# Optimization experiments

Hardware: AMD Instinct MI355X
Metric: run time of the kernel (lower is better)

The kernel has to match this reference:

```python
import jax, jax.numpy as jnp
import numpy as np

B, T = 8, 32
DSENS, DA = 512, 32
DS = DE = DIM = 128  # dim_structure = dim_encoded_sensory = memory dim


def l2norm(x, eps=1e-12):
    return x / jnp.maximum(jnp.linalg.norm(x, axis=-1, keepdims=True), eps)


def mlp3(x, W1, b1, W2, b2, W3, b3):
    h = jax.nn.relu(x @ W1 + b1)
    h = jax.nn.relu(h @ W2 + b2)
    return h @ W3 + b3


def mse(a, b):
    return jnp.mean((a - b) ** 2)


def assoc_scan(x, gate, prev):
    # h_t = gate_t * h_{t-1} + x_t with h_0 = prev.  x:[b,t,w], gate:[b,t,1], prev:[b,w]
    x = x.at[:, 0].add(gate[:, 0] * prev)
    def combine(ca, cb):
        ga, xa = ca
        gb, xb = cb
        return ga * gb, xb + gb * xa
    _, h = jax.lax.associative_scan(combine, (gate, x), axis=1)
    return h


def _forward(sensory, actions, enc_w, dec_w, pi_w1, pi_b1, pi_w2, pi_b2, pi_w3, pi_b3,
             rnn_init_hidden, wq, wk, wv, w_hp, m_w1, m_b1, m_w2, m_b2, m_w3, m_b3,
             o_w1, o_b1, o_w2, o_b2, o_w3, o_b3, v_w1, v_b1, v_w2, v_b2, v_w3, v_b3,
             integration_ratio):
    b, t = actions.shape[:2]
    # --- path integration: action MLP -> per-step transition matrices -> sequential RNN scan ---
    trans = mlp3(actions, pi_w1, pi_b1, pi_w2, pi_b2, pi_w3, pi_b3).reshape(b, t, DS, DS)
    h0 = jnp.broadcast_to(l2norm(rnn_init_hidden)[0], (b, DS))
    def step(h, Tm):
        h = l2norm(jax.nn.relu(jnp.einsum('bi,bij->bj', h, Tm)))
        return h, h
    _, hs = jax.lax.scan(step, h0, jnp.moveaxis(trans, 1, 0))
    structural = jnp.moveaxis(hs, 0, 1)                      # [b,t,DS]

    enc = sensory @ enc_w                                    # [b,t,DE]
    meta_p = (m_w1, m_b1, m_w2, m_b2, m_w3, m_b3)

    def retrieve(s, e):
        q = jnp.concatenate([s, e], axis=-1) @ wq            # to_queries
        r = mlp3(q, *meta_p)                                 # meta_memory_mlp (slow copy)
        d = mlp3(r, o_w1, o_b1, o_w2, o_b2, o_w3, o_b3)      # memory_output_decoder
        return d[..., :DS], d[..., DS:]

    dec_gen_s, dec_enc = retrieve(structural, jnp.zeros_like(enc))
    gen_loss = mse(sensory, dec_enc @ dec_w)
    dec_s2, _ = retrieve(jnp.zeros_like(structural), enc)
    relational_loss = 2.0 * mse(dec_s2, structural)          # source computes the identical loss twice
    corr_s, corr_e = retrieve(dec_gen_s, enc)
    sse = jnp.sum((corr_e - enc) ** 2, axis=-1, keepdims=True)
    pred_var = mlp3(jnp.concatenate([corr_s, dec_gen_s, sse], axis=-1),
                    v_w1, v_b1, v_w2, v_b2, v_w3, v_b3)
    inf_s = dec_gen_s + (corr_s - dec_gen_s) * jax.nn.sigmoid(integration_ratio) * pred_var
    consistency_loss = mse(dec_gen_s, inf_s)
    final_s, inf_e = retrieve(inf_s, jnp.zeros_like(enc))
    inf_loss = mse(sensory, inf_e @ dec_w)

    # --- test-time-training memory write: per-sample meta-grads + two assoc scans ---
    joint = jnp.concatenate([final_s, enc], axis=-1)         # [b,t,2*DS]
    keys, values = joint @ wk, joint @ wv                    # [b,t,DIM]
    hp = joint @ w_hp                                        # [b,t,3]
    lr, forget, beta = hp[..., 0], hp[..., 1], hp[..., 2]

    def meta_loss(p, k, v):
        return jnp.mean((mlp3(k, *p) - v) ** 2)
    pb = tuple(jnp.broadcast_to(p, (b,) + p.shape) for p in meta_p)
    grads = jax.vmap(jax.vmap(jax.grad(meta_loss), in_axes=(None, 0, 0)))(pb, keys, values)
    G = jnp.concatenate([g.reshape(b, t, -1) for g in grads], axis=-1)  # [b,t,Wtot]
    W = G.shape[-1]
    p_flat = jnp.broadcast_to(jnp.concatenate([p.ravel() for p in meta_p])[None], (b, W))
    update = assoc_scan(G * lr[..., None], jax.nn.sigmoid(beta)[..., None],
                        jnp.zeros((b, W), G.dtype))          # momentum scan
    acc = assoc_scan(-update, jax.nn.sigmoid(forget)[..., None], p_flat)  # weight-decay scan
    next_state = jnp.concatenate([acc[:, -1], update[:, -1]], axis=-1)    # [b,2W]

    total = gen_loss + relational_loss + consistency_loss + inf_loss
    return jnp.concatenate([jnp.reshape(total, (1,)), next_state.ravel()])


def setup_inputs() -> dict:
    key = jax.random.key(0)
    ks = iter(jax.random.split(key, 48))
    def rn(shape, s=1.0):
        return jax.random.normal(next(ks), shape, dtype=jnp.float32) * s
    def lin(fi, fo):
        return rn((fi, fo), 1.0 / np.sqrt(fi))
    z = lambda n: jnp.zeros((n,), jnp.float32)
    return {
        "sensory": rn((B, T, DSENS)),
        "actions": rn((B, T, DA)),
        "enc_w": lin(DSENS, DE), "dec_w": lin(DE, DSENS),
        "pi_w1": lin(DA, 4 * DA), "pi_b1": z(4 * DA),
        "pi_w2": lin(4 * DA, 4 * DA), "pi_b2": z(4 * DA),
        "pi_w3": lin(4 * DA, DS * DS), "pi_b3": z(DS * DS),
        "rnn_init_hidden": rn((1, DS), 0.01),
        "wq": lin(DS + DE, DIM), "wk": lin(DS + DE, DIM), "wv": lin(DS + DE, DIM),
        "w_hp": lin(DS + DE, 3),
        "m_w1": lin(DIM, 2 * DIM), "m_b1": z(2 * DIM),
        "m_w2": lin(2 * DIM, 2 * DIM), "m_b2": z(2 * DIM),
        "m_w3": lin(2 * DIM, DIM), "m_b3": z(DIM),
        "o_w1": lin(DIM, 2 * DIM), "o_b1": z(2 * DIM),
        "o_w2": lin(2 * DIM, 2 * DIM), "o_b2": z(2 * DIM),
        "o_w3": lin(2 * DIM, DS + DE), "o_b3": z(DS + DE),
        "v_w1": lin(2 * DS + 1, 2 * DS), "v_b1": z(2 * DS),
        "v_w2": lin(2 * DS, 2 * DS), "v_b2": z(2 * DS),
        "v_w3": lin(2 * DS, DS), "v_b3": z(DS),
        "integration_ratio": jnp.zeros((), jnp.float32),
    }


def reference(sensory, actions, enc_w, dec_w, pi_w1, pi_b1, pi_w2, pi_b2, pi_w3, pi_b3,
              rnn_init_hidden, wq, wk, wv, w_hp, m_w1, m_b1, m_w2, m_b2, m_w3, m_b3,
              o_w1, o_b1, o_w2, o_b2, o_w3, o_b3, v_w1, v_b1, v_w2, v_b2, v_w3, v_b3,
              integration_ratio):
    return _forward(sensory, actions, enc_w, dec_w, pi_w1, pi_b1, pi_w2, pi_b2, pi_w3, pi_b3,
                    rnn_init_hidden, wq, wk, wv, w_hp, m_w1, m_b1, m_w2, m_b2, m_w3, m_b3,
                    o_w1, o_b1, o_w2, o_b2, o_w3, o_b3, v_w1, v_b1, v_w2, v_b2, v_w3, v_b3,
                    integration_ratio)
```

## Files before the change

kernel.cpp:

```cpp
#include <hip/hip_runtime.h>
#include <cstdint>
#include <cstddef>

#define DEV __device__ __forceinline__

constexpr size_t W_TOT = 131712;
constexpr size_t OFF_W1 = 0;
constexpr size_t OFF_B1 = 32768;
constexpr size_t OFF_W2 = 33024;
constexpr size_t OFF_B2 = 98560;
constexpr size_t OFF_W3 = 98816;
constexpr size_t OFF_B3 = 131584;

constexpr int OPS = 272;

constexpr size_t P_LOSS = 0;
constexpr size_t P_WA   = 1024;
constexpr size_t P_WU   = 1280;
constexpr size_t P_FT   = 1536;
constexpr size_t P_HP   = 2048;
constexpr size_t P_H2PI = 4096;
constexpr size_t P_ENC  = P_H2PI + 32768;
constexpr size_t P_DGS  = P_ENC + 32768;
constexpr size_t P_INF  = P_DGS + 32768;
constexpr size_t P_KEYS = P_INF + 32768;
constexpr size_t P_VALS = P_KEYS + 32768;
constexpr size_t P_D3   = P_VALS + 32768;
constexpr size_t P_H1   = P_D3 + 32768;
constexpr size_t P_H2   = P_H1 + 65536;
constexpr size_t P_D1   = P_H2 + 65536;
constexpr size_t P_D2   = P_D1 + 65536;
constexpr size_t P_STRUCT = P_D2 + 65536;
constexpr size_t P_TRANS  = P_STRUCT + 32768;

DEV float sigm(float x) { return 1.f / (1.f + expf(-x)); }

DEV float wgsum256(float v, float* red) {
#pragma unroll
  for (int s = 32; s > 0; s >>= 1) v += __shfl_xor(v, s);
  if ((threadIdx.x & 63) == 0) red[threadIdx.x >> 6] = v;
  __syncthreads();
  const float t = red[0] + red[1] + red[2] + red[3];
  __syncthreads();
  return t;
}

DEV float wgsum512(float v, float* red) {
#pragma unroll
  for (int s = 32; s > 0; s >>= 1) v += __shfl_xor(v, s);
  if ((threadIdx.x & 63) == 0) red[threadIdx.x >> 6] = v;
  __syncthreads();
  float t = 0.f;
#pragma unroll
  for (int w = 0; w < 8; ++w) t += red[w];
  __syncthreads();
  return t;
}

template<int K, int OUT, int ROWS>
DEV void dense512(const float* __restrict__ W, const float* __restrict__ bias,
                  const float* in, int ips, float* out, int ops, int relu,
                  float* scr)
{
  constexpr int OUTG = OUT / 4;
  constexpr int NSEG = 512 / OUTG;
  constexpr int KS   = K / NSEG;
  constexpr int NG   = KS / 8;
  static_assert(K % NSEG == 0 && KS % 8 == 0 && NG >= 1, "bad shape");
  const int tid = (int)threadIdx.x;
  const int c   = tid & (OUTG - 1);
  const int seg = tid / OUTG;
  const int k0  = seg * KS;
  const float4* W4 = reinterpret_cast<const float4*>(W);
  float4 w0[8], w1[8];
  float acc[ROWS][4];
#pragma unroll
  for (int r = 0; r < ROWS; ++r) {
    acc[r][0] = 0.f; acc[r][1] = 0.f; acc[r][2] = 0.f; acc[r][3] = 0.f;
  }
#pragma unroll
  for (int u = 0; u < 8; ++u) w0[u] = W4[(size_t)(k0 + u) * OUTG + c];
#pragma unroll
  for (int t = 1; t <= NG; ++t) {
    if (t < NG) {
#pragma unroll
      for (int u = 0; u < 8; ++u) w1[u] = W4[(size_t)(k0 + t * 8 + u) * OUTG + c];
    }
#pragma unroll
    for (int u = 0; u < 8; ++u) {
      const int kk = k0 + (t - 1) * 8 + u;
#pragma unroll
      for (int r = 0; r < ROWS; ++r) {
        const float x = in[r * ips + kk];
        acc[r][0] = fmaf(x, w0[u].x, acc[r][0]);
        acc[r][1] = fmaf(x, w0[u].y, acc[r][1]);
        acc[r][2] = fmaf(x, w0[u].z, acc[r][2]);
        acc[r][3] = fmaf(x, w0[u].w, acc[r][3]);
      }
    }
    if (t < NG) {
#pragma unroll
      for (int u = 0; u < 8; ++u) w0[u] = w1[u];
    }
  }
  float4* s4 = reinterpret_cast<float4*>(scr);
#pragma unroll
  for (int r = 0; r < ROWS; ++r)
    s4[(seg * ROWS + r) * OUTG + c] =
        make_float4(acc[r][0], acc[r][1], acc[r][2], acc[r][3]);
  __syncthreads();
  for (int idx = tid; idx < OUT * ROWS; idx += 512) {
    const int r = idx / OUT, j = idx % OUT;
    float v = (bias ? bias[j] : 0.f);
#pragma unroll
    for (int s = 0; s < NSEG; ++s) v += scr[(s * ROWS + r) * OUT + j];
    if (relu) v = fmaxf(v, 0.f);
    out[r * ops + j] = v;
  }
  __syncthreads();
}

template<int K, int OUT, int ROWS>
DEV void denseW(const float* __restrict__ W, const float* __restrict__ bias,
                const float* in, int ips, float* out, int ops, int relu,
                float* scr)
{
  constexpr int OUTG = OUT / 4;
  constexpr int HALF = OUTG / 2;
  constexpr int TPS  = HALF;
  constexpr int NSEG = 256 / TPS;
  constexpr int KS   = K / NSEG;
  constexpr int NG   = KS / 8;
  static_assert(KS % 8 == 0 && NG >= 1, "bad shape");
  const int tid = (int)threadIdx.x;
  const int c   = tid & (TPS - 1);
  const int seg = tid / TPS;
  const int k0  = seg * KS;
  const float4* W4 = reinterpret_cast<const float4*>(W);
  float4 a0[8], b0[8], a1[8], b1[8];
  float acc[ROWS][8];
#pragma unroll
  for (int r = 0; r < ROWS; ++r)
#pragma unroll
    for (int x = 0; x < 8; ++x) acc[r][x] = 0.f;
#pragma unroll
  for (int u = 0; u < 8; ++u) {
    a0[u] = W4[(size_t)(k0 + u) * OUTG + c];
    b0[u] = W4[(size_t)(k0 + u) * OUTG + c + HALF];
  }
#pragma unroll
  for (int t = 1; t <= NG; ++t) {
    if (t < NG) {
#pragma unroll
      for (int u = 0; u < 8; ++u) {
        a1[u] = W4[(size_t)(k0 + t * 8 + u) * OUTG + c];
        b1[u] = W4[(size_t)(k0 + t * 8 + u) * OUTG + c + HALF];
      }
    }
#pragma unroll
    for (int u = 0; u < 8; ++u) {
      const int kk = k0 + (t - 1) * 8 + u;
#pragma unroll
      for (int r = 0; r < ROWS; ++r) {
        const float x = in[r * ips + kk];
        acc[r][0] = fmaf(x, a0[u].x, acc[r][0]);
        acc[r][1] = fmaf(x, a0[u].y, acc[r][1]);
        acc[r][2] = fmaf(x, a0[u].z, acc[r][2]);
        acc[r][3] = fmaf(x, a0[u].w, acc[r][3]);
        acc[r][4] = fmaf(x, b0[u].x, acc[r][4]);
        acc[r][5] = fmaf(x, b0[u].y, acc[r][5]);
        acc[r][6] = fmaf(x, b0[u].z, acc[r][6]);
        acc[r][7] = fmaf(x, b0[u].w, acc[r][7]);
      }
    }
    if (t < NG) {
#pragma unroll
      for (int u = 0; u < 8; ++u) { a0[u] = a1[u]; b0[u] = b1[u]; }
    }
  }
  float4* s4 = reinterpret_cast<float4*>(scr);
#pragma unroll
  for (int r = 0; r < ROWS; ++r) {
    s4[(seg * ROWS + r) * OUTG + c] =
        make_float4(acc[r][0], acc[r][1], acc[r][2], acc[r][3]);
    s4[(seg * ROWS + r) * OUTG + c + HALF] =
        make_float4(acc[r][4], acc[r][5], acc[r][6], acc[r][7]);
  }
  __syncthreads();
  for (int idx = tid; idx < OUT * ROWS; idx += 256) {
    const int r = idx / OUT, j = idx % OUT;
    float v = (bias ? bias[j] : 0.f);
#pragma unroll
    for (int s = 0; s < NSEG; ++s) v += scr[(s * ROWS + r) * OUT + j];
    if (relu) v = fmaxf(v, 0.f);
    out[r * ops + j] = v;
  }
  __syncthreads();
}

__global__ __launch_bounds__(128) void k_pi_h2(
    const float* __restrict__ actions,
    const float* __restrict__ w1, const float* __restrict__ b1,
    const float* __restrict__ w2, const float* __restrict__ b2,
    float* __restrict__ h2out)
{
  const int row = blockIdx.x;
  const int j = threadIdx.x;
  __shared__ float a[32];
  __shared__ float h1[128];
  if (j < 32) a[j] = actions[row * 32 + j];
  __syncthreads();
  float acc = b1[j];
#pragma unroll
  for (int i = 0; i < 32; ++i) acc = fmaf(a[i], w1[i * 128 + j], acc);
  h1[j] = fmaxf(acc, 0.f);
  __syncthreads();
  float acc2 = b2[j];
#pragma unroll 8
  for (int i = 0; i < 128; ++i) acc2 = fmaf(h1[i], w2[i * 128 + j], acc2);
  h2out[row * 128 + j] = fmaxf(acc2, 0.f);
}

__global__ __launch_bounds__(256) void k_pi_trans(
    const float* __restrict__ h2,
    const float* __restrict__ w3, const float* __restrict__ b3,
    float* __restrict__ trans)
{
  const int col = blockIdx.x * 256 + threadIdx.x;
  const int r0 = blockIdx.y * 32;
  __shared__ float h2s[32][128];
  for (int idx = threadIdx.x; idx < 32 * 128; idx += 256)
    h2s[idx >> 7][idx & 127] = h2[(size_t)(r0 + (idx >> 7)) * 128 + (idx & 127)];
  __syncthreads();
  float acc[32];
#pragma unroll
  for (int r = 0; r < 32; ++r) acc[r] = 0.f;
  float w0[8], w1[8];
#pragma unroll
  for (int c = 0; c < 8; ++c) w0[c] = w3[(size_t)c * 16384 + col];
#pragma unroll
  for (int i = 8; i <= 128; i += 8) {
    if (i < 128) {
#pragma unroll
      for (int c = 0; c < 8; ++c) w1[c] = w3[(size_t)(i + c) * 16384 + col];
    }
#pragma unroll
    for (int r = 0; r < 32; ++r) {
      float s = acc[r];
#pragma unroll
      for (int c = 0; c < 8; ++c) s = fmaf(h2s[r][i - 8 + c], w0[c], s);
      acc[r] = s;
    }
    if (i < 128) {
#pragma unroll
      for (int c = 0; c < 8; ++c) w0[c] = w1[c];
    }
  }
  const float bv = b3[col];
#pragma unroll
  for (int r = 0; r < 32; ++r)
    trans[(size_t)(r0 + r) * 16384 + col] = acc[r] + bv;
}

__global__ __launch_bounds__(1024) void k_rnn(
    const float* __restrict__ trans, const float* __restrict__ rinit,
    float* __restrict__ structural)
{
  const int b = blockIdx.x;
  const int tid = threadIdx.x;
  const int j = tid & 127, seg = tid >> 7;
  __shared__ float h[128];
  __shared__ float part[8][128];
  if (tid < 64) {
    const float x0 = rinit[tid], x1 = rinit[tid + 64];
    float ss = x0 * x0 + x1 * x1;
#pragma unroll
    for (int s = 32; s > 0; s >>= 1) ss += __shfl_xor(ss, s);
    const float iv = 1.f / fmaxf(sqrtf(ss), 1e-12f);
    h[tid] = x0 * iv;
    h[tid + 64] = x1 * iv;
  }
  __syncthreads();

  float cur[16], nxt[16];
  {
    const float* T0 = trans + ((size_t)(b * 32) << 14);
#pragma unroll
    for (int k = 0; k < 16; ++k) cur[k] = T0[(size_t)(seg * 16 + k) * 128 + j];
  }
  for (int t = 0; t < 32; ++t) {
    if (t < 31) {
      const float* Tn = trans + ((size_t)(b * 32 + t + 1) << 14);
#pragma unroll
      for (int k = 0; k < 16; ++k) nxt[k] = Tn[(size_t)(seg * 16 + k) * 128 + j];
    }
    float acc = 0.f;
#pragma unroll
    for (int k = 0; k < 16; ++k) acc = fmaf(h[seg * 16 + k], cur[k], acc);
    part[seg][j] = acc;
    __syncthreads();
    if (tid < 64) {
      const int l = tid;
      float r0 = part[0][l], r1 = part[0][l + 64];
#pragma unroll
      for (int s = 1; s < 8; ++s) { r0 += part[s][l]; r1 += part[s][l + 64]; }
      r0 = fmaxf(r0, 0.f);
      r1 = fmaxf(r1, 0.f);
      float ss = r0 * r0 + r1 * r1;
#pragma unroll
      for (int s = 32; s > 0; s >>= 1) ss += __shfl_xor(ss, s);
      const float iv = 1.f / fmaxf(sqrtf(ss), 1e-12f);
      const float v0 = r0 * iv, v1 = r1 * iv;
      h[l] = v0;
      h[l + 64] = v1;
      structural[(size_t)(b * 32 + t) * 128 + l] = v0;
      structural[(size_t)(b * 32 + t) * 128 + l + 64] = v1;
    }
    __syncthreads();
    if (t < 31) {
#pragma unroll
      for (int k = 0; k < 16; ++k) cur[k] = nxt[k];
    }
  }
}

__global__ __launch_bounds__(512) void kA(
    const float* __restrict__ sensory, const float* __restrict__ structural_,
    const float* __restrict__ enc_w, const float* __restrict__ wq,
    const float* __restrict__ dec_w,
    const float* __restrict__ mw1, const float* __restrict__ mb1,
    const float* __restrict__ mw2, const float* __restrict__ mb2,
    const float* __restrict__ mw3, const float* __restrict__ mb3,
    const float* __restrict__ ow1, const float* __restrict__ ob1,
    const float* __restrict__ ow2, const float* __restrict__ ob2,
    const float* __restrict__ ow3, const float* __restrict__ ob3,
    float* __restrict__ ws_enc, float* __restrict__ ws_dgs,
    float* __restrict__ lossPart)
{
  const int g = blockIdx.x, tid = threadIdx.x;
  __shared__ float sens[512], sRow[128], eRow[128];
  __shared__ float actA[2 * OPS], actB[2 * OPS];
  __shared__ float4 scr4buf[1024];
  __shared__ float red[8];
  float* scr = reinterpret_cast<float*>(scr4buf);

  sens[tid] = sensory[(size_t)g * 512 + tid];
  if (tid < 128) sRow[tid] = structural_[(size_t)g * 128 + tid];
  __syncthreads();

  dense512<512, 128, 1>(enc_w, nullptr, sens, 0, eRow, 0, 0, scr);
  if (tid < 128) ws_enc[(size_t)g * 128 + tid] = eRow[tid];

  dense512<128, 128, 1>(wq, nullptr, sRow, 0, actA, 0, 0, scr);
  dense512<128, 128, 1>(wq + 128 * 128, nullptr, eRow, 0, actA + OPS, 0, 0, scr);
  dense512<128, 256, 2>(mw1, mb1, actA, OPS, actB, OPS, 1, scr);
  dense512<256, 256, 2>(mw2, mb2, actB, OPS, actA, OPS, 1, scr);
  dense512<256, 128, 2>(mw3, mb3, actA, OPS, actB, OPS, 0, scr);
  dense512<128, 256, 2>(ow1, ob1, actB, OPS, actA, OPS, 1, scr);
  dense512<256, 256, 2>(ow2, ob2, actA, OPS, actB, OPS, 1, scr);
  dense512<256, 256, 2>(ow3, ob3, actB, OPS, actA, OPS, 0, scr);
  float lrel = 0.f;
  if (tid < 128) {
    ws_dgs[(size_t)g * 128 + tid] = actA[tid];
    const float d = actA[OPS + tid] - sRow[tid];
    lrel = d * d;
  }
  const float relT = wgsum512(lrel, red);
  if (tid == 0) lossPart[256 + g] = relT;
  dense512<128, 512, 1>(dec_w, nullptr, &actA[128], 0, actB, 0, 0, scr);
  {
    const float d = actB[tid] - sens[tid];
    const float genT = wgsum512(d * d, red);
    if (tid == 0) lossPart[g] = genT;
  }
}

__global__ __launch_bounds__(512) void kB(
    const float* __restrict__ ws_enc, const float* __restrict__ ws_dgs,
    const float* __restrict__ wq,
    const float* __restrict__ mw1, const float* __restrict__ mb1,
    const float* __restrict__ mw2, const float* __restrict__ mb2,
    const float* __restrict__ mw3, const float* __restrict__ mb3,
    const float* __restrict__ ow1, const float* __restrict__ ob1,
    const float* __restrict__ ow2, const float* __restrict__ ob2,
    const float* __restrict__ ow3, const float* __restrict__ ob3,
    const float* __restrict__ vw1, const float* __restrict__ vb1,
    const float* __restrict__ vw2, const float* __restrict__ vb2,
    const float* __restrict__ vw3, const float* __restrict__ vb3,
    const float* __restrict__ ir,
    float* __restrict__ ws_inf, float* __restrict__ lossPart)
{
  const int g = blockIdx.x, tid = threadIdx.x;
  __shared__ float eRow[128], dgsRow[128], cRow[128];
  __shared__ float cbuf[256];
  __shared__ float actA[2 * OPS], actB[2 * OPS];
  __shared__ float4 scr4buf[1024];
  __shared__ float red[8];
  float* scr = reinterpret_cast<float*>(scr4buf);

  if (tid < 128) eRow[tid] = ws_enc[(size_t)g * 128 + tid];
  else if (tid < 256) dgsRow[tid - 128] = ws_dgs[(size_t)g * 128 + (tid - 128)];
  __syncthreads();

  if (tid < 256) cbuf[tid] = (tid < 128) ? dgsRow[tid] : eRow[tid - 128];
  __syncthreads();
  dense512<256, 128, 1>(wq, nullptr, cbuf, 0, actA, 0, 0, scr);
  dense512<128, 256, 1>(mw1, mb1, actA, 0, actB, 0, 1, scr);
  dense512<256, 256, 1>(mw2, mb2, actB, 0, actA, 0, 1, scr);
  dense512<256, 128, 1>(mw3, mb3, actA, 0, actB, 0, 0, scr);
  dense512<128, 256, 1>(ow1, ob1, actB, 0, actA, 0, 1, scr);
  dense512<256, 256, 1>(ow2, ob2, actA, 0, actB, 0, 1, scr);
  dense512<256, 256, 1>(ow3, ob3, actB, 0, actA, 0, 0, scr);
  float ls = 0.f;
  if (tid < 128) {
    cRow[tid] = actA[tid];
    const float d = actA[128 + tid] - eRow[tid];
    ls = d * d;
  }
  const float sseV = wgsum512(ls, red);

  if (tid < 256) cbuf[tid] = (tid < 128) ? cRow[tid] : dgsRow[tid - 128];
  __syncthreads();
  dense512<256, 256, 1>(vw1, vb1, cbuf, 0, actB, 0, 0, scr);
  if (tid < 256)
    actB[tid] = fmaxf(actB[tid] + sseV * vw1[(size_t)256 * 256 + tid], 0.f);
  __syncthreads();
  dense512<256, 256, 1>(vw2, vb2, actB, 0, actA, 0, 1, scr);
  dense512<256, 128, 1>(vw3, vb3, actA, 0, actB, 0, 0, scr);
  const float sig = sigm(ir[0]);
  float lc = 0.f;
  if (tid < 128) {
    const float diff = (cRow[tid] - dgsRow[tid]) * sig * actB[tid];
    ws_inf[(size_t)g * 128 + tid] = dgsRow[tid] + diff;
    lc = diff * diff;
  }
  const float consT = wgsum512(lc, red);
  if (tid == 0) lossPart[512 + g] = consT;
}

__global__ __launch_bounds__(512) void kC(
    const float* __restrict__ sensory,
    const float* __restrict__ ws_enc, const float* __restrict__ ws_inf,
    const float* __restrict__ wq, const float* __restrict__ dec_w,
    const float* __restrict__ mw1, const float* __restrict__ mb1,
    const float* __restrict__ mw2, const float* __restrict__ mb2,
    const float* __restrict__ mw3, const float* __restrict__ mb3,
    const float* __restrict__ ow1, const float* __restrict__ ob1,
    const float* __restrict__ ow2, const float* __restrict__ ob2,
    const float* __restrict__ ow3, const float* __restrict__ ob3,
    const float* __restrict__ wk, const float* __restrict__ wv,
    const float* __restrict__ w_hp,
    float* __restrict__ gKeys, float* __restrict__ gVals,
    float* __restrict__ gHp, float* __restrict__ lossPart)
{
  const int g = blockIdx.x, tid = threadIdx.x;
  __shared__ float sens[512], eRow[128], infRow[128];
  __shared__ float cbuf[256];
  __shared__ float actA[2 * OPS], actB[2 * OPS];
  __shared__ float4 scr4buf[1024];
  __shared__ float red[8];
  float* scr = reinterpret_cast<float*>(scr4buf);

  sens[tid] = sensory[(size_t)g * 512 + tid];
  if (tid < 128) eRow[tid] = ws_enc[(size_t)g * 128 + tid];
  else if (tid < 256) infRow[tid - 128] = ws_inf[(size_t)g * 128 + (tid - 128)];
  __syncthreads();

  dense512<128, 128, 1>(wq, nullptr, infRow, 0, actA, 0, 0, scr);
  dense512<128, 256, 1>(mw1, mb1, actA, 0, actB, 0, 1, scr);
  dense512<256, 256, 1>(mw2, mb2, actB, 0, actA, 0, 1, scr);
  dense512<256, 128, 1>(mw3, mb3, actA, 0, actB, 0, 0, scr);
  dense512<128, 256, 1>(ow1, ob1, actB, 0, actA, 0, 1, scr);
  dense512<256, 256, 1>(ow2, ob2, actA, 0, actB, 0, 1, scr);
  dense512<256, 256, 1>(ow3, ob3, actB, 0, actA, 0, 0, scr);
  dense512<128, 512, 1>(dec_w, nullptr, &actA[128], 0, actB, 0, 0, scr);
  {
    const float d = actB[tid] - sens[tid];
    const float infT = wgsum512(d * d, red);
    if (tid == 0) lossPart[768 + g] = infT;
  }
  __syncthreads();

  if (tid < 256) cbuf[tid] = (tid < 128) ? actA[tid] : eRow[tid - 128];
  __syncthreads();
  dense512<256, 128, 1>(wk, nullptr, cbuf, 0, gKeys + (size_t)g * 128, 0, 0, scr);
  dense512<256, 128, 1>(wv, nullptr, cbuf, 0, gVals + (size_t)g * 128, 0, 0, scr);
  const int c = tid >> 6, l = tid & 63;
  float acc = 0.f;
  if (c < 3) {
    for (int i = l; i < 256; i += 64)
      acc = fmaf(cbuf[i], w_hp[i * 3 + c], acc);
  }
#pragma unroll
  for (int s = 32; s > 0; s >>= 1) acc += __shfl_xor(acc, s);
  if (c < 3 && l == 0) gHp[(size_t)g * 4 + c] = acc;
}

__global__ __launch_bounds__(256) void kD(
    const float* __restrict__ gKeys, const float* __restrict__ gVals,
    const float* __restrict__ gHp,
    const float* __restrict__ mw1, const float* __restrict__ mb1,
    const float* __restrict__ mw2, const float* __restrict__ mb2,
    const float* __restrict__ mw3, const float* __restrict__ mb3,
    float* __restrict__ ws_h1, float* __restrict__ ws_h2,
    float* __restrict__ ws_d1, float* __restrict__ ws_d2, float* __restrict__ ws_d3,
    float* __restrict__ wA, float* __restrict__ wU, float* __restrict__ Ft)
{
  const int tid = threadIdx.x;
  __shared__ float kRow[128], vRow[128];
  __shared__ float actA[256], actB[256], d3R[128], d2R[256];
  __shared__ float4 scr4buf[1024];
  __shared__ float lr[256], sf[256], sb[256];
  float* scr = reinterpret_cast<float*>(scr4buf);
  if (blockIdx.x == 256) {
    lr[tid] = gHp[(size_t)tid * 4 + 0];
    sf[tid] = sigm(gHp[(size_t)tid * 4 + 1]);
    sb[tid] = sigm(gHp[(size_t)tid * 4 + 2]);
    __syncthreads();
    if (tid < 8) {
      const int b = tid;
      float cB = 1.f, cF = 1.f, Bv = 1.f;
      wU[b * 32 + 31] = lr[b * 32 + 31];
      wA[b * 32 + 31] = lr[b * 32 + 31];
      for (int t = 30; t >= 0; --t) {
        cB = sb[b * 32 + t + 1] * cB;
        cF = sf[b * 32 + t + 1] * cF;
        Bv = cF + sb[b * 32 + t + 1] * Bv;
        wU[b * 32 + t] = lr[b * 32 + t] * cB;
        wA[b * 32 + t] = lr[b * 32 + t] * Bv;
      }
      float ft = 1.f;
      for (int t = 0; t < 32; ++t) ft *= sf[b * 32 + t];
      Ft[b] = ft;
    }
    return;
  }
  const int g = blockIdx.x;
  if (tid < 128) kRow[tid] = gKeys[(size_t)g * 128 + tid];
  else vRow[tid - 128] = gVals[(size_t)g * 128 + (tid - 128)];
  __syncthreads();
  denseW<128, 256, 1>(mw1, mb1, kRow, 0, actA, 0, 1, scr);
  ws_h1[(size_t)g * 256 + tid] = actA[tid];
  denseW<256, 256, 1>(mw2, mb2, actA, 0, actB, 0, 1, scr);
  ws_h2[(size_t)g * 256 + tid] = actB[tid];
  denseW<256, 128, 1>(mw3, mb3, actB, 0, d3R, 0, 0, scr);
  if (tid < 128) {
    const float d = (d3R[tid] - vRow[tid]) * (2.f / 128.f);
    d3R[tid] = d;
    ws_d3[(size_t)g * 128 + tid] = d;
  }
  __syncthreads();
  {
    const int j = tid;
    float acc = 0.f;
    for (int jc = 0; jc < 128; jc += 4) {
      const float4 w = *reinterpret_cast<const float4*>(&mw3[(size_t)j * 128 + jc]);
      acc = fmaf(w.x, d3R[jc + 0], acc);
      acc = fmaf(w.y, d3R[jc + 1], acc);
      acc = fmaf(w.z, d3R[jc + 2], acc);
      acc = fmaf(w.w, d3R[jc + 3], acc);
    }
    const float v = (actB[j] > 0.f) ? acc : 0.f;
    d2R[j] = v;
    ws_d2[(size_t)g * 256 + j] = v;
  }
  __syncthreads();
  {
    const int j = tid;
    float acc = 0.f;
    for (int jc = 0; jc < 256; jc += 4) {
      const float4 w = *reinterpret_cast<const float4*>(&mw2[(size_t)j * 256 + jc]);
      acc = fmaf(w.x, d2R[jc + 0], acc);
      acc = fmaf(w.y, d2R[jc + 1], acc);
      acc = fmaf(w.z, d2R[jc + 2], acc);
      acc = fmaf(w.w, d2R[jc + 3], acc);
    }
    ws_d1[(size_t)g * 256 + j] = (actA[j] > 0.f) ? acc : 0.f;
  }
}

DEV void outer_body(const float* __restrict__ L, int Lld,
                    const float* __restrict__ D, int Dld,
                    const float* __restrict__ P,
                    const float* __restrict__ wA, const float* __restrict__ wU,
                    const float* __restrict__ Ftot,
                    float* __restrict__ out, size_t regionOff, int J,
                    int b, int i0, float* __restrict__ wAk, float* __restrict__ wUk)
{
  const int tid = threadIdx.x;
  for (int idx = tid; idx < 1024; idx += 256) {
    const int t = idx >> 5, ii = idx & 31;
    const float kv = L[(size_t)(b * 32 + t) * Lld + i0 + ii];
    wAk[t * 33 + ii] = wA[b * 32 + t] * kv;
    wUk[t * 33 + ii] = wU[b * 32 + t] * kv;
  }
  __syncthreads();
  const int j = (J == 256) ? tid : (tid & 127);
  const int g2 = (J == 256) ? 0 : (tid >> 7);
  const int span = (J == 256) ? 32 : 16;
  const int iBeg = g2 * span;
  float dv[32];
#pragma unroll
  for (int t = 0; t < 32; ++t) dv[t] = D[(size_t)(b * 32 + t) * Dld + j];
  const float ft = Ftot[b];
  float* ob = out + 1 + (size_t)b * (2 * W_TOT);
  for (int ii = iBeg; ii < iBeg + span; ++ii) {
    float aA = 0.f, aU = 0.f;
#pragma unroll
    for (int t = 0; t < 32; ++t) {
      aA = fmaf(wAk[t * 33 + ii], dv[t], aA);
      aU = fmaf(wUk[t * 33 + ii], dv[t], aU);
    }
    const int i = i0 + ii;
    const size_t w = regionOff + (size_t)i * J + j;
    ob[w] = ft * P[(size_t)i * J + j] - aA;
    ob[W_TOT + w] = aU;
  }
}

__global__ __launch_bounds__(256) void kW(
    const float* __restrict__ keys, const float* __restrict__ h1,
    const float* __restrict__ h2, const float* __restrict__ d1,
    const float* __restrict__ d2, const float* __restrict__ d3,
    const float* __restrict__ mw1, const float* __restrict__ mb1,
    const float* __restrict__ mw2, const float* __restrict__ mb2,
    const float* __restrict__ mw3, const float* __restrict__ mb3,
    const float* __restrict__ wA, const float* __restrict__ wU,
    const float* __restrict__ Ft, const float* __restrict__ lossPart,
    float* __restrict__ out)
{
  __shared__ float wAk[32 * 33], wUk[32 * 33];
  __shared__ float red[4];
  const int bid = blockIdx.x;
  const int tid = threadIdx.x;
  if (bid < 32) {
    outer_body(keys, 128, d1, 256, mw1, wA, wU, Ft, out, OFF_W1, 256,
               bid >> 2, (bid & 3) * 32, wAk, wUk);
  } else if (bid < 96) {
    const int x = bid - 32;
    outer_body(h1, 256, d2, 256, mw2, wA, wU, Ft, out, OFF_W2, 256,
               x >> 3, (x & 7) * 32, wAk, wUk);
  } else if (bid < 160) {
    const int x = bid - 96;
    outer_body(h2, 256, d3, 128, mw3, wA, wU, Ft, out, OFF_W3, 128,
               x >> 3, (x & 7) * 32, wAk, wUk);
  } else if (bid < 168) {
    const int b = bid - 160;
    const float ft = Ft[b];
    float* ob = out + 1 + (size_t)b * (2 * W_TOT);
    for (int idx = tid; idx < 640; idx += 256) {
      const float* D; int ld, j; size_t off; float pv;
      if (idx < 256)      { D = d1; ld = 256; j = idx;       off = OFF_B1; pv = mb1[j]; }
      else if (idx < 512) { D = d2; ld = 256; j = idx - 256; off = OFF_B2; pv = mb2[j]; }
      else                { D = d3; ld = 128; j = idx - 512; off = OFF_B3; pv = mb3[j]; }
      float aA = 0.f, aU = 0.f;
#pragma unroll
      for (int t = 0; t < 32; ++t) {
        const float dv = D[(size_t)(b * 32 + t) * ld + j];
        aA = fmaf(wA[b * 32 + t], dv, aA);
        aU = fmaf(wU[b * 32 + t], dv, aU);
      }
      ob[off + j] = ft * pv - aA;
      ob[W_TOT + off + j] = aU;
    }
  } else {
    const int c = tid >> 6, l = tid & 63;
    float v = lossPart[c * 256 + l] + lossPart[c * 256 + 64 + l] +
              lossPart[c * 256 + 128 + l] + lossPart[c * 256 + 192 + l];
#pragma unroll
    for (int s = 32; s > 0; s >>= 1) v += __shfl_xor(v, s);
    if (l == 0) red[c] = v;
    __syncthreads();
    if (tid == 0) {
      const float i1 = 1.f / (256.f * 512.f);
      const float i2 = 1.f / (256.f * 128.f);
      out[0] = red[0] * i1 + 2.f * red[1] * i2 + red[2] * i2 + red[3] * i1;
    }
  }
}

extern "C" void kernel_launch(void* const* d_in, const int* in_sizes, int n_in,
                              void* d_out, int out_size, void* d_ws, size_t ws_size,
                              hipStream_t stream)
{
  const float* sensory = (const float*)d_in[0];
  const float* actions = (const float*)d_in[1];
  const float* enc_w = (const float*)d_in[2];
  const float* dec_w = (const float*)d_in[3];
  const float* pi_w1 = (const float*)d_in[4];
  const float* pi_b1 = (const float*)d_in[5];
  const float* pi_w2 = (const float*)d_in[6];
  const float* pi_b2 = (const float*)d_in[7];
  const float* pi_w3 = (const float*)d_in[8];
  const float* pi_b3 = (const float*)d_in[9];
  const float* rinit = (const float*)d_in[10];
  const float* wq = (const float*)d_in[11];
  const float* wk = (const float*)d_in[12];
  const float* wv = (const float*)d_in[13];
  const float* w_hp = (const float*)d_in[14];
  const float* mw1 = (const float*)d_in[15]; const float* mb1 = (const float*)d_in[16];
  const float* mw2 = (const float*)d_in[17]; const float* mb2 = (const float*)d_in[18];
  const float* mw3 = (const float*)d_in[19]; const float* mb3 = (const float*)d_in[20];
  const float* ow1 = (const float*)d_in[21]; const float* ob1 = (const float*)d_in[22];
  const float* ow2 = (const float*)d_in[23]; const float* ob2 = (const float*)d_in[24];
  const float* ow3 = (const float*)d_in[25]; const float* ob3 = (const float*)d_in[26];
  const float* vw1 = (const float*)d_in[27]; const float* vb1 = (const float*)d_in[28];
  const float* vw2 = (const float*)d_in[29]; const float* vb2 = (const float*)d_in[30];
  const float* vw3 = (const float*)d_in[31]; const float* vb3 = (const float*)d_in[32];
  const float* ir  = (const float*)d_in[33];

  float* ws  = (float*)d_ws;
  float* out = (float*)d_out;

  float* lossP = ws + P_LOSS;
  float* wA = ws + P_WA; float* wU = ws + P_WU; float* Ft = ws + P_FT;
  float* hp = ws + P_HP;
  float* h2pi = ws + P_H2PI;
  float* enc = ws + P_ENC;
  float* dgs = ws + P_DGS;
  float* inf = ws + P_INF;
  float* keys = ws + P_KEYS;
  float* vals = ws + P_VALS;
  float* d3s = ws + P_D3;
  float* h1s = ws + P_H1;
  float* h2s = ws + P_H2;
  float* d1s = ws + P_D1;
  float* d2s = ws + P_D2;
  float* structural = ws + P_STRUCT;
  float* trans = ws + P_TRANS;

  hipLaunchKernelGGL(k_pi_h2, dim3(256), dim3(128), 0, stream,
                     actions, pi_w1, pi_b1, pi_w2, pi_b2, h2pi);
  hipLaunchKernelGGL(k_pi_trans, dim3(64, 8), dim3(256), 0, stream,
                     h2pi, pi_w3, pi_b3, trans);
  hipLaunchKernelGGL(k_rnn, dim3(8), dim3(1024), 0, stream, trans, rinit, structural);
  hipLaunchKernelGGL(kA, dim3(256), dim3(512), 0, stream,
                     sensory, structural, enc_w, wq, dec_w,
                     mw1, mb1, mw2, mb2, mw3, mb3,
                     ow1, ob1, ow2, ob2, ow3, ob3,
                     enc, dgs, lossP);
  hipLaunchKernelGGL(kB, dim3(256), dim3(512), 0, stream,
                     enc, dgs, wq,
                     mw1, mb1, mw2, mb2, mw3, mb3,
                     ow1, ob1, ow2, ob2, ow3, ob3,
                     vw1, vb1, vw2, vb2, vw3, vb3,
                     ir, inf, lossP);
  hipLaunchKernelGGL(kC, dim3(256), dim3(512), 0, stream,
                     sensory, enc, inf, wq, dec_w,
                     mw1, mb1, mw2, mb2, mw3, mb3,
                     ow1, ob1, ow2, ob2, ow3, ob3,
                     wk, wv, w_hp, keys, vals, hp, lossP);
  hipLaunchKernelGGL(kD, dim3(257), dim3(256), 0, stream,
                     keys, vals, hp, mw1, mb1, mw2, mb2, mw3, mb3,
                     h1s, h2s, d1s, d2s, d3s, wA, wU, Ft);
  hipLaunchKernelGGL(kW, dim3(169), dim3(256), 0, stream,
                     keys, h1s, h2s, d1s, d2s, d3s,
                     mw1, mb1, mw2, mb2, mw3, mb3,
                     wA, wU, Ft, lossP, out);
}
```

Before: 185.8 us.

## Fuse correction and inference kernels and linearize pi_trans grid with batch-major order

Merges kernels kB and kC into one kernel kBC. The inferred row is kept in shared memory instead of being written to and reread from a global workspace buffer. This removes one launch and the global round trip, at the cost of a longer kernel that holds more shared memory per block. Separately, k_pi_trans now uses a 1D grid whose block index interleaves the batch, so blocks launched together share the same weight columns, which may improve L2 reuse of w3.

```diff
diff --git a/kernel.cpp b/kernel.cpp
--- a/kernel.cpp
+++ b/kernel.cpp
@@ -22,8 +22,7 @@
 constexpr size_t P_H2PI = 4096;
 constexpr size_t P_ENC  = P_H2PI + 32768;
 constexpr size_t P_DGS  = P_ENC + 32768;
-constexpr size_t P_INF  = P_DGS + 32768;
-constexpr size_t P_KEYS = P_INF + 32768;
+constexpr size_t P_KEYS = P_DGS + 32768;
 constexpr size_t P_VALS = P_KEYS + 32768;
 constexpr size_t P_D3   = P_VALS + 32768;
 constexpr size_t P_H1   = P_D3 + 32768;
@@ -34,16 +33,6 @@
 constexpr size_t P_TRANS  = P_STRUCT + 32768;
 
 DEV float sigm(float x) { return 1.f / (1.f + expf(-x)); }
-
-DEV float wgsum256(float v, float* red) {
-#pragma unroll
-  for (int s = 32; s > 0; s >>= 1) v += __shfl_xor(v, s);
-  if ((threadIdx.x & 63) == 0) red[threadIdx.x >> 6] = v;
-  __syncthreads();
-  const float t = red[0] + red[1] + red[2] + red[3];
-  __syncthreads();
-  return t;
-}
 
 DEV float wgsum512(float v, float* red) {
 #pragma unroll
@@ -226,8 +215,10 @@
     const float* __restrict__ w3, const float* __restrict__ b3,
     float* __restrict__ trans)
 {
-  const int col = blockIdx.x * 256 + threadIdx.x;
-  const int r0 = blockIdx.y * 32;
+  const int batch = blockIdx.x & 7;
+  const int colblk = blockIdx.x >> 3;
+  const int col = colblk * 256 + threadIdx.x;
+  const int r0 = batch * 32;
   __shared__ float h2s[32][128];
   for (int idx = threadIdx.x; idx < 32 * 128; idx += 256)
     h2s[idx >> 7][idx & 127] = h2[(size_t)(r0 + (idx >> 7)) * 128 + (idx & 127)];
@@ -375,9 +366,10 @@
   }
 }
 
-__global__ __launch_bounds__(512) void kB(
+__global__ __launch_bounds__(512) void kBC(
+    const float* __restrict__ sensory,
     const float* __restrict__ ws_enc, const float* __restrict__ ws_dgs,
-    const float* __restrict__ wq,
+    const float* __restrict__ wq, const float* __restrict__ dec_w,
     const float* __restrict__ mw1, const float* __restrict__ mb1,
     const float* __restrict__ mw2, const float* __restrict__ mb2,
     const float* __restrict__ mw3, const float* __restrict__ mb3,
@@ -387,17 +379,20 @@
     const float* __restrict__ vw1, const float* __restrict__ vb1,
     const float* __restrict__ vw2, const float* __restrict__ vb2,
     const float* __restrict__ vw3, const float* __restrict__ vb3,
-    const float* __restrict__ ir,
-    float* __restrict__ ws_inf, float* __restrict__ lossPart)
+    const float* __restrict__ wk, const float* __restrict__ wv,
+    const float* __restrict__ w_hp, const float* __restrict__ ir,
+    float* __restrict__ gKeys, float* __restrict__ gVals,
+    float* __restrict__ gHp, float* __restrict__ lossPart)
 {
   const int g = blockIdx.x, tid = threadIdx.x;
-  __shared__ float eRow[128], dgsRow[128], cRow[128];
+  __shared__ float sens[512], eRow[128], dgsRow[128], cRow[128], infRow[128];
   __shared__ float cbuf[256];
   __shared__ float actA[2 * OPS], actB[2 * OPS];
   __shared__ float4 scr4buf[1024];
   __shared__ float red[8];
   float* scr = reinterpret_cast<float*>(scr4buf);
 
+  sens[tid] = sensory[(size_t)g * 512 + tid];
   if (tid < 128) eRow[tid] = ws_enc[(size_t)g * 128 + tid];
   else if (tid < 256) dgsRow[tid - 128] = ws_dgs[(size_t)g * 128 + (tid - 128)];
   __syncthreads();
@@ -431,39 +426,11 @@
   float lc = 0.f;
   if (tid < 128) {
     const float diff = (cRow[tid] - dgsRow[tid]) * sig * actB[tid];
-    ws_inf[(size_t)g * 128 + tid] = dgsRow[tid] + diff;
+    infRow[tid] = dgsRow[tid] + diff;
     lc = diff * diff;
   }
   const float consT = wgsum512(lc, red);
   if (tid == 0) lossPart[512 + g] = consT;
-}
-
-__global__ __launch_bounds__(512) void kC(
-    const float* __restrict__ sensory,
-    const float* __restrict__ ws_enc, const float* __restrict__ ws_inf,
-    const float* __restrict__ wq, const float* __restrict__ dec_w,
-    const float* __restrict__ mw1, const float* __restrict__ mb1,
-    const float* __restrict__ mw2, const float* __restrict__ mb2,
-    const float* __restrict__ mw3, const float* __restrict__ mb3,
-    const float* __restrict__ ow1, const float* __restrict__ ob1,
-    const float* __restrict__ ow2, const float* __restrict__ ob2,
-    const float* __restrict__ ow3, const float* __restrict__ ob3,
-    const float* __restrict__ wk, const float* __restrict__ wv,
-    const float* __restrict__ w_hp,
-    float* __restrict__ gKeys, float* __restrict__ gVals,
-    float* __restrict__ gHp, float* __restrict__ lossPart)
-{
-  const int g = blockIdx.x, tid = threadIdx.x;
-  __shared__ float sens[512], eRow[128], infRow[128];
-  __shared__ float cbuf[256];
-  __shared__ float actA[2 * OPS], actB[2 * OPS];
-  __shared__ float4 scr4buf[1024];
-  __shared__ float red[8];
-  float* scr = reinterpret_cast<float*>(scr4buf);
-
-  sens[tid] = sensory[(size_t)g * 512 + tid];
-  if (tid < 128) eRow[tid] = ws_enc[(size_t)g * 128 + tid];
-  else if (tid < 256) infRow[tid - 128] = ws_inf[(size_t)g * 128 + (tid - 128)];
   __syncthreads();
 
   dense512<128, 128, 1>(wq, nullptr, infRow, 0, actA, 0, 0, scr);
@@ -718,7 +685,6 @@
   float* h2pi = ws + P_H2PI;
   float* enc = ws + P_ENC;
   float* dgs = ws + P_DGS;
-  float* inf = ws + P_INF;
   float* keys = ws + P_KEYS;
   float* vals = ws + P_VALS;
   float* d3s = ws + P_D3;
@@ -731,7 +697,7 @@
 
   hipLaunchKernelGGL(k_pi_h2, dim3(256), dim3(128), 0, stream,
                      actions, pi_w1, pi_b1, pi_w2, pi_b2, h2pi);
-  hipLaunchKernelGGL(k_pi_trans, dim3(64, 8), dim3(256), 0, stream,
+  hipLaunchKernelGGL(k_pi_trans, dim3(512), dim3(256), 0, stream,
                      h2pi, pi_w3, pi_b3, trans);
   hipLaunchKernelGGL(k_rnn, dim3(8), dim3(1024), 0, stream, trans, rinit, structural);
   hipLaunchKernelGGL(kA, dim3(256), dim3(512), 0, stream,
@@ -739,17 +705,12 @@
                      mw1, mb1, mw2, mb2, mw3, mb3,
                      ow1, ob1, ow2, ob2, ow3, ob3,
                      enc, dgs, lossP);
-  hipLaunchKernelGGL(kB, dim3(256), dim3(512), 0, stream,
-                     enc, dgs, wq,
+  hipLaunchKernelGGL(kBC, dim3(256), dim3(512), 0, stream,
+                     sensory, enc, dgs, wq, dec_w,
                      mw1, mb1, mw2, mb2, mw3, mb3,
                      ow1, ob1, ow2, ob2, ow3, ob3,
                      vw1, vb1, vw2, vb2, vw3, vb3,
-                     ir, inf, lossP);
-  hipLaunchKernelGGL(kC, dim3(256), dim3(512), 0, stream,
-                     sensory, enc, inf, wq, dec_w,
-                     mw1, mb1, mw2, mb2, mw3, mb3,
-                     ow1, ob1, ow2, ob2, ow3, ob3,
-                     wk, wv, w_hp, keys, vals, hp, lossP);
+                     wk, wv, w_hp, ir, keys, vals, hp, lossP);
   hipLaunchKernelGGL(kD, dim3(257), dim3(256), 0, stream,
                      keys, vals, hp, mw1, mb1, mw2, mb2, mw3, mb3,
                      h1s, h2s, d1s, d2s, d3s, wA, wU, Ft);
```

Result: slower. 220.0 us (+18.4%).
